# Kernel optimization log

Measured on AMD Instinct MI355X. Metric: run time of the kernel, lower is better.

The kernel has to match this reference:

```python
import jax, jax.numpy as jnp
import numpy as np

N = 100000          # total nodes
E = 3200000         # total edges (avg degree 32)
B = 100             # num graphs
NPG = N // B        # nodes per graph (uniform -> to_dense_batch is a reshape)
D_IN, D_H, D_E, N_CLS = 128, 64, 32, 10


def setup_inputs() -> dict:
    key = jax.random.key(0)
    ks = jax.random.split(key, 12)
    x = jax.random.normal(ks[0], (N, D_IN), jnp.float32)
    # edges strictly within each graph: offset by graph block
    epg = E // B
    offs = (jnp.arange(E, dtype=jnp.int32) // epg) * NPG
    src = jax.random.randint(ks[1], (E,), 0, NPG, jnp.int32) + offs
    dst = jax.random.randint(ks[2], (E,), 0, NPG, jnp.int32) + offs
    edge_index = jnp.stack([src, dst])
    batch = jnp.repeat(jnp.arange(B, dtype=jnp.int32), NPG)

    def glorot(k, fi, fo):
        return jax.random.normal(k, (fi, fo), jnp.float32) * (1.0 / np.sqrt(fi))

    return {
        "x": x, "edge_index": edge_index, "batch": batch,
        "W_a1": glorot(ks[3], D_IN, D_H), "b_a1": jnp.zeros((D_H,), jnp.float32),
        "W_a2": glorot(ks[4], D_H, D_E),  "b_a2": jnp.zeros((D_E,), jnp.float32),
        "W_x1": glorot(ks[5], D_IN, D_H), "b_x1": jnp.zeros((D_H,), jnp.float32),
        "W_x2": glorot(ks[6], D_H, D_E),  "b_x2": jnp.zeros((D_E,), jnp.float32),
        "W_lin": glorot(ks[7], D_E * D_E, N_CLS),
        "b_lin": jnp.zeros((N_CLS,), jnp.float32),
    }


def _gcn(x, W, b, src, dst, n):
    """PyG GCNConv(improved=True): sym-norm with self-loop weight 2."""
    h = x @ W                                                   # [n, out]
    deg = jax.ops.segment_sum(jnp.ones_like(dst, h.dtype), dst, n) + 2.0
    dinv = jax.lax.rsqrt(deg)                                   # [n]
    coef = dinv[src] * dinv[dst]                                # [E]
    agg = jax.ops.segment_sum(h[src] * coef[:, None], dst, n)   # gather-scatter
    agg = agg + (2.0 * dinv * dinv)[:, None] * h                # self-loop term
    return agg + b


def _segment_softmax(v, seg, nseg):
    m = jax.ops.segment_max(v, seg, nseg)
    e = jnp.exp(v - m[seg])
    s = jax.ops.segment_sum(e, seg, nseg)
    return e / s[seg]


def reference(x, edge_index, batch, W_a1, b_a1, W_a2, b_a2,
              W_x1, b_x1, W_x2, b_x2, W_lin, b_lin):
    src, dst = edge_index[0], edge_index[1]
    n = x.shape[0]
    a1 = jax.nn.relu(_gcn(x, W_a1, b_a1, src, dst, n))
    a2 = _segment_softmax(_gcn(a1, W_a2, b_a2, src, dst, n), batch, B)
    x1 = jax.nn.relu(_gcn(x, W_x1, b_x1, src, dst, n))
    x2 = jax.nn.relu(_gcn(x1, W_x2, b_x2, src, dst, n))
    # uniform graph sizes -> to_dense_batch is a reshape (no padding needed)
    a_b = a2.reshape(B, NPG, D_E)
    x_b = x2.reshape(B, NPG, D_E)
    prods = jnp.einsum('bne,bnf->bef', a_b, x_b)   # bmm(a^T, x): [B, D_E, D_E]
    flat = prods.reshape(B, D_E * D_E)
    return jax.nn.softmax(flat @ W_lin + b_lin, axis=-1)
```

## Files before the change

kernel.cpp:

```cpp
#include <hip/hip_runtime.h>
#include <hip/hip_bf16.h>
#include <hip/hip_fp16.h>

#define N_NODES 100000
#define N_EDGES 3200000
#define NB      100
#define NPG     1000
#define EPG     32000
#define DIN     128
#define DH      64
#define DE      32
#define NCLS    10
#define SORT_BLOCKS 104


typedef _Float16 h2_t __attribute__((ext_vector_type(2)));

__device__ __forceinline__ float dot2f(unsigned a, unsigned b, float c) {
#if __has_builtin(__builtin_amdgcn_fdot2)
    return __builtin_amdgcn_fdot2(__builtin_bit_cast(h2_t, a),
                                  __builtin_bit_cast(h2_t, b), c, false);
#else
    float d;
    asm("v_dot2_f32_f16 %0, %1, %2, %3" : "=v"(d) : "v"(a), "v"(b), "v"(c));
    return d;
#endif
}

#define DOT8(rA, rB, dv)                                                        \
    acc[0] = dot2f(__builtin_amdgcn_perm(rB.x, rA.x, 0x05040100u), dv, acc[0]); \
    acc[1] = dot2f(__builtin_amdgcn_perm(rB.x, rA.x, 0x07060302u), dv, acc[1]); \
    acc[2] = dot2f(__builtin_amdgcn_perm(rB.y, rA.y, 0x05040100u), dv, acc[2]); \
    acc[3] = dot2f(__builtin_amdgcn_perm(rB.y, rA.y, 0x07060302u), dv, acc[3]); \
    acc[4] = dot2f(__builtin_amdgcn_perm(rB.z, rA.z, 0x05040100u), dv, acc[4]); \
    acc[5] = dot2f(__builtin_amdgcn_perm(rB.z, rA.z, 0x07060302u), dv, acc[5]); \
    acc[6] = dot2f(__builtin_amdgcn_perm(rB.w, rA.w, 0x05040100u), dv, acc[6]); \
    acc[7] = dot2f(__builtin_amdgcn_perm(rB.w, rA.w, 0x07060302u), dv, acc[7]);


union SharedU {
    struct {
        __align__(16) unsigned short buf[EPG];
        int cnt[NPG];
        int pre[NPG];
        int sm[1024];
        unsigned short dh[NPG];
    } so;
    struct {
        float xs[4][32][128];
        float ws[32][128];
    } ge;
};

__global__ __launch_bounds__(1024) void k_sg(const int* __restrict__ src,
                                             const int* __restrict__ dst,
                                             const float* __restrict__ x,
                                             const float* __restrict__ Wa,
                                             const float* __restrict__ Wx,
                                             int* __restrict__ rowptr,
                                             float* __restrict__ dinv,
                                             unsigned int* __restrict__ esrc,
                                             unsigned short* __restrict__ h16) {
    __shared__ SharedU S;
    int t = threadIdx.x;
    if (blockIdx.x < SORT_BLOCKS) {
        int g = (blockIdx.x & 7) + 8 * (blockIdx.x >> 3);
        if (g >= NB) return;
        int ebase = g * EPG, nbase = g * NPG;
        if (t < NPG) S.so.cnt[t] = 0;
        __syncthreads();
        for (int i = t; i < EPG; i += 1024)
            atomicAdd(&S.so.cnt[dst[ebase + i] - nbase], 1);
        __syncthreads();
        int v = (t < NPG) ? S.so.cnt[t] : 0;
        if (t < NPG) {
            float dv = rsqrtf((float)v + 2.0f);
            dinv[nbase + t] = dv;
            S.so.dh[t] = __half_as_ushort(__float2half_rn(dv));
        }
        S.so.sm[t] = v;
        __syncthreads();
        for (int off = 1; off < 1024; off <<= 1) {
            int xx = (t >= off) ? S.so.sm[t - off] : 0;
            __syncthreads();
            S.so.sm[t] += xx;
            __syncthreads();
        }
        if (t < NPG) {
            int ex = S.so.sm[t] - v;
            S.so.pre[t] = ex;
            rowptr[nbase + t] = ebase + ex;
        }
        if (g == NB - 1 && t == 0) rowptr[N_NODES] = N_EDGES;
        __syncthreads();
        for (int i = t; i < EPG; i += 1024) {
            int e = ebase + i;
            int d = dst[e] - nbase;
            int s = src[e] - nbase;
            int pos = atomicAdd(&S.so.pre[d], 1);
            S.so.buf[pos] = (unsigned short)s;
        }
        __syncthreads();
        uint4* gout = (uint4*)(esrc + ebase);
        const ushort4* lbuf = (const ushort4*)S.so.buf;
        for (int i = t; i < EPG / 4; i += 1024) {
            ushort4 s4 = lbuf[i];
            uint4 o;
            o.x = ((unsigned)s4.x * 16) | ((unsigned)S.so.dh[s4.x] << 16);
            o.y = ((unsigned)s4.y * 16) | ((unsigned)S.so.dh[s4.y] << 16);
            o.z = ((unsigned)s4.z * 16) | ((unsigned)S.so.dh[s4.z] << 16);
            o.w = ((unsigned)s4.w * 16) | ((unsigned)S.so.dh[s4.w] << 16);
            gout[i] = o;
        }
    } else {
        int b = blockIdx.x - SORT_BLOCKS;
        int xcd = b & 7, slot = b >> 3;
        int g = xcd + 8 * (slot >> 3);
        int chunk = slot & 7;
        if (g >= NB) return;
        int q  = t >> 8;
        int tq = t & 255;
        int row0 = g * NPG + chunk * 128 + q * 32;
        for (int i = 0; i < 4; i++) {
            int idx = tq + 256 * i;
            int r = idx >> 5, k4 = idx & 31;
            int rr = row0 + r; if (rr >= N_NODES) rr = N_NODES - 1;
            *(float4*)&S.ge.xs[q][r][k4 * 4] = *(const float4*)&x[(size_t)rr * 128 + k4 * 4];
        }
        float acc[4][4] = {};
        int rg = tq >> 5, cg = tq & 31;
        for (int kt = 0; kt < 4; kt++) {
            __syncthreads();
            {
                int kk = t >> 5, c4 = t & 31;
                int k = kt * 32 + kk, c = c4 * 4;
                float4 v;
                if (c < 64) v = *(const float4*)&Wa[k * 64 + c];
                else        v = *(const float4*)&Wx[k * 64 + (c - 64)];
                *(float4*)&S.ge.ws[kk][c] = v;
            }
            __syncthreads();
            for (int kk = 0; kk < 32; kk++) {
                float4 w = *(float4*)&S.ge.ws[kk][cg * 4];
                float xv[4];
                for (int i = 0; i < 4; i++) xv[i] = S.ge.xs[q][rg * 4 + i][kt * 32 + kk];
                for (int i = 0; i < 4; i++) {
                    acc[i][0] += xv[i] * w.x; acc[i][1] += xv[i] * w.y;
                    acc[i][2] += xv[i] * w.z; acc[i][3] += xv[i] * w.w;
                }
            }
        }
        for (int i = 0; i < 4; i++) {
            int r = row0 + rg * 4 + i;
            if (r < N_NODES) {
                union { ushort4 u; __half2 h[2]; } pk;
                pk.h[0] = __floats2half2_rn(acc[i][0], acc[i][1]);
                pk.h[1] = __floats2half2_rn(acc[i][2], acc[i][3]);
                *(ushort4*)&h16[r * 128 + cg * 4] = pk.u;
            }
        }
    }
}


__global__ __launch_bounds__(256) void k_agg128(const unsigned short* __restrict__ h16,
                                                const int* __restrict__ rowptr,
                                                const unsigned int* __restrict__ esrc,
                                                const float* __restrict__ dinv,
                                                const float* __restrict__ ba,
                                                const float* __restrict__ bx,
                                                unsigned short* __restrict__ outB16) {
    int xcd = blockIdx.x & 7, slot = blockIdx.x >> 3;
    int gi = slot / 250, chunk = slot - gi * 250;
    int g = xcd + 8 * gi;
    if (g >= NB) return;
    int nl   = chunk * 4 + (threadIdx.x >> 6);
    int wid  = g * NPG + nl;
    int lane = threadIdx.x & 63;
    int sub = lane >> 4;
    int cl  = lane & 15;
    const uint4* hg4 = (const uint4*)(h16 + g * NPG * 128);
    float acc[8] = {};
    union U8 { uint4 u; __half h[8]; };
    int e0 = rowptr[wid], e1 = rowptr[wid + 1];
    int e = e0;
    for (; e + 16 <= e1; e += 16) {
        unsigned pv0 = esrc[e + sub];
        unsigned pv1 = esrc[e + 4 + sub];
        unsigned pv2 = esrc[e + 8 + sub];
        unsigned pv3 = esrc[e + 12 + sub];
        uint4 r0 = hg4[(pv0 & 0xffffu) + cl];
        uint4 r1 = hg4[(pv1 & 0xffffu) + cl];
        uint4 r2 = hg4[(pv2 & 0xffffu) + cl];
        uint4 r3 = hg4[(pv3 & 0xffffu) + cl];
        unsigned dA = __builtin_amdgcn_perm(pv1, pv0, 0x07060302u);
        unsigned dB = __builtin_amdgcn_perm(pv3, pv2, 0x07060302u);
        DOT8(r0, r1, dA);
        DOT8(r2, r3, dB);
    }
    for (; e + 8 <= e1; e += 8) {
        unsigned pv0 = esrc[e + sub];
        unsigned pv1 = esrc[e + 4 + sub];
        uint4 r0 = hg4[(pv0 & 0xffffu) + cl];
        uint4 r1 = hg4[(pv1 & 0xffffu) + cl];
        unsigned dA = __builtin_amdgcn_perm(pv1, pv0, 0x07060302u);
        DOT8(r0, r1, dA);
    }
    for (; e < e1; e += 4) {
        int ee = e + sub;
        unsigned pv; float scale;
        if (ee < e1) { pv = esrc[ee]; scale = 1.0f; }
        else         { pv = esrc[e];  scale = 0.0f; }
        U8 r; r.u = hg4[(pv & 0xffffu) + cl];
        float dv = scale * __half2float(__ushort_as_half((unsigned short)(pv >> 16)));
        #pragma unroll
        for (int k = 0; k < 8; k++)
            acc[k] += dv * __half2float(r.h[k]);
    }
    #pragma unroll
    for (int k = 0; k < 8; k++) {
        acc[k] += __shfl_xor(acc[k], 16);
        acc[k] += __shfl_xor(acc[k], 32);
    }
    if (sub == 0) {
        float di = dinv[wid];
        float sw = 2.0f * di * di;
        U8 hv; hv.u = hg4[nl * 16 + cl];
        int cl8 = cl * 8;
        const float* bb = (cl8 < 64) ? &ba[cl8] : &bx[cl8 - 64];
        union { __half2 h[4]; uint4 q; } pk;
        #pragma unroll
        for (int k = 0; k < 4; k++) {
            float ox = fmaxf(di * acc[2 * k]     + sw * __half2float(hv.h[2 * k])     + bb[2 * k],     0.0f);
            float oy = fmaxf(di * acc[2 * k + 1] + sw * __half2float(hv.h[2 * k + 1]) + bb[2 * k + 1], 0.0f);
            pk.h[k] = __floats2half2_rn(ox, oy);
        }
        *(uint4*)&outB16[wid * 128 + cl8] = pk.q;
    }
}


__global__ __launch_bounds__(256) void k_agg64(const unsigned short* __restrict__ g16,
                                               const int* __restrict__ rowptr,
                                               const unsigned int* __restrict__ esrc,
                                               const float* __restrict__ dinv,
                                               const float* __restrict__ ba2,
                                               const float* __restrict__ bx2,
                                               float* __restrict__ s2) {
    int xcd = blockIdx.x & 7, slot = blockIdx.x >> 3;
    int gi = slot / 250, chunk = slot - gi * 250;
    int g = xcd + 8 * gi;
    if (g >= NB) return;
    int nl   = chunk * 4 + (threadIdx.x >> 6);
    int wid  = g * NPG + nl;
    int lane = threadIdx.x & 63;
    int sub = lane >> 3;
    int cl  = lane & 7;
    const uint4* gg4 = (const uint4*)(g16 + g * NPG * 64);
    float acc[8] = {};
    union U8 { uint4 u; __half h[8]; };
    int e0 = rowptr[wid], e1 = rowptr[wid + 1];
    int e = e0;
    for (; e + 16 <= e1; e += 16) {
        unsigned pv0 = esrc[e + sub];
        unsigned pv1 = esrc[e + 8 + sub];
        uint4 r0 = gg4[((pv0 & 0xffffu) >> 1) + cl];
        uint4 r1 = gg4[((pv1 & 0xffffu) >> 1) + cl];
        unsigned dA = __builtin_amdgcn_perm(pv1, pv0, 0x07060302u);
        DOT8(r0, r1, dA);
    }
    for (; e < e1; e += 8) {
        int ee = e + sub;
        unsigned pv; float scale;
        if (ee < e1) { pv = esrc[ee]; scale = 1.0f; }
        else         { pv = esrc[e];  scale = 0.0f; }
        U8 r; r.u = gg4[((pv & 0xffffu) >> 1) + cl];
        float dv = scale * __half2float(__ushort_as_half((unsigned short)(pv >> 16)));
        #pragma unroll
        for (int k = 0; k < 8; k++)
            acc[k] += dv * __half2float(r.h[k]);
    }
    #pragma unroll
    for (int k = 0; k < 8; k++) {
        acc[k] += __shfl_xor(acc[k], 8);
        acc[k] += __shfl_xor(acc[k], 16);
        acc[k] += __shfl_xor(acc[k], 32);
    }
    if (sub == 0) {
        float di = dinv[wid];
        float sw = 2.0f * di * di;
        U8 hv; hv.u = gg4[nl * 8 + cl];
        int cl8 = cl * 8;
        float o[8];
        #pragma unroll
        for (int k = 0; k < 8; k++)
            o[k] = di * acc[k] + sw * __half2float(hv.h[k]);
        if (cl8 < 32) {
            #pragma unroll
            for (int k = 0; k < 8; k++) o[k] += ba2[cl8 + k];
        } else {
            #pragma unroll
            for (int k = 0; k < 8; k++) o[k] = fmaxf(o[k] + bx2[cl8 - 32 + k], 0.0f);
        }
        *(float4*)&s2[wid * 64 + cl8]     = make_float4(o[0], o[1], o[2], o[3]);
        *(float4*)&s2[wid * 64 + cl8 + 4] = make_float4(o[4], o[5], o[6], o[7]);
    }
}


__global__ __launch_bounds__(256) void k_gemm2(const unsigned short* __restrict__ Bm16,
                                               const float* __restrict__ Wa2,
                                               const float* __restrict__ Wx2,
                                               unsigned short* __restrict__ g16) {
    __shared__ float xs[64][132];
    __shared__ float ws[64][68];
    int xcd = blockIdx.x & 7, slot = blockIdx.x >> 3;
    int g = xcd + 8 * (slot >> 4);
    int chunk = slot & 15;
    if (g >= NB) return;
    int row0 = g * NPG + chunk * 64;
    int t = threadIdx.x;
    for (int i = 0; i < 4; i++) {
        int idx = t + 256 * i;
        int k = idx >> 4, c4 = idx & 15, c = c4 * 4;
        float4 v;
        if (c < 32) v = *(const float4*)&Wa2[k * 32 + c];
        else        v = *(const float4*)&Wx2[k * 32 + (c - 32)];
        *(float4*)&ws[k][c] = v;
    }
    for (int i = 0; i < 4; i++) {
        int idx = t + 256 * i;
        int r = idx >> 4, c8 = idx & 15;
        int rr = row0 + r; if (rr >= N_NODES) rr = N_NODES - 1;
        union { uint4 u; __half2 h[4]; } pk;
        pk.u = *(const uint4*)&Bm16[rr * 128 + c8 * 8];
        float2 f0 = __half22float2(pk.h[0]);
        float2 f1 = __half22float2(pk.h[1]);
        float2 f2 = __half22float2(pk.h[2]);
        float2 f3 = __half22float2(pk.h[3]);
        int cb = c8 * 8;
        *(float4*)&xs[r][cb]     = make_float4(f0.x, f0.y, f1.x, f1.y);
        *(float4*)&xs[r][cb + 4] = make_float4(f2.x, f2.y, f3.x, f3.y);
    }
    __syncthreads();
    int cg = t & 15, rg = t >> 4;
    int koff = (cg < 8) ? 0 : 64;
    float acc[4][4] = {};
    for (int k = 0; k < 64; k++) {
        float4 w = *(float4*)&ws[k][cg * 4];
        float xv[4];
        for (int i = 0; i < 4; i++) xv[i] = xs[rg * 4 + i][koff + k];
        for (int i = 0; i < 4; i++) {
            acc[i][0] += xv[i] * w.x; acc[i][1] += xv[i] * w.y;
            acc[i][2] += xv[i] * w.z; acc[i][3] += xv[i] * w.w;
        }
    }
    for (int i = 0; i < 4; i++) {
        int r = row0 + rg * 4 + i;
        if (r < N_NODES) {
            union { ushort4 u; __half2 h[2]; } pk;
            pk.h[0] = __floats2half2_rn(acc[i][0], acc[i][1]);
            pk.h[1] = __floats2half2_rn(acc[i][2], acc[i][3]);
            *(ushort4*)&g16[r * 64 + cg * 4] = pk.u;
        }
    }
}


__global__ __launch_bounds__(512) void k_smax(const float* __restrict__ s2,
                                              float* __restrict__ gmax,
                                              float* __restrict__ sinv) {
    __shared__ float red[16][32];
    int g = (blockIdx.x & 7) + 8 * (blockIdx.x >> 3);
    if (g >= NB) return;
    int t = threadIdx.x;
    int c = t & 31, sub = t >> 5;
    size_t base = (size_t)g * NPG;
    float m = -1e30f;
    for (int n = sub; n < NPG; n += 16)
        m = fmaxf(m, s2[(base + n) * 64 + c]);
    red[sub][c] = m; __syncthreads();
    if (sub == 0) {
        for (int j = 1; j < 16; j++) m = fmaxf(m, red[j][c]);
        red[0][c] = m;
        gmax[g * 32 + c] = m;
    }
    __syncthreads();
    m = red[0][c];
    __syncthreads();
    float sum = 0.0f;
    for (int n = sub; n < NPG; n += 16)
        sum += __expf(s2[(base + n) * 64 + c] - m);
    red[sub][c] = sum; __syncthreads();
    if (sub == 0) {
        for (int j = 1; j < 16; j++) sum += red[j][c];
        sinv[g * 32 + c] = 1.0f / sum;
    }
}


__global__ __launch_bounds__(256) void k_pool(const float* __restrict__ s2,
                                              const float* __restrict__ gmax,
                                              float* __restrict__ prods) {
    __shared__ float ta[25][32];
    __shared__ float tx[25][32];
    __shared__ float gm[32];
    int xcd = blockIdx.x & 7, slot = blockIdx.x >> 3;
    int g = xcd + 8 * (slot >> 3);
    int ch = slot & 7;
    if (g >= NB) return;
    int t = threadIdx.x;
    if (t < 32) gm[t] = gmax[g * 32 + t];
    int e  = t >> 3;
    int f4 = t & 7;
    float a0 = 0.f, a1 = 0.f, a2 = 0.f, a3 = 0.f;
    int base = g * NPG + ch * 125;
    for (int n0 = 0; n0 < 125; n0 += 25) {
        __syncthreads();
        for (int i = t; i < 25 * 16; i += 256) {
            int r = i >> 4, c4 = i & 15;
            float4 v = *(const float4*)&s2[(size_t)(base + n0 + r) * 64 + c4 * 4];
            if (c4 < 8) {
                int cb = c4 * 4;
                v.x = __expf(v.x - gm[cb + 0]);
                v.y = __expf(v.y - gm[cb + 1]);
                v.z = __expf(v.z - gm[cb + 2]);
                v.w = __expf(v.w - gm[cb + 3]);
                *(float4*)&ta[r][cb] = v;
            } else {
                *(float4*)&tx[r][(c4 - 8) * 4] = v;
            }
        }
        __syncthreads();
        #pragma unroll 5
        for (int n = 0; n < 25; n++) {
            float a   = ta[n][e];
            float4 xv = *(float4*)&tx[n][f4 * 4];
            a0 += a * xv.x; a1 += a * xv.y; a2 += a * xv.z; a3 += a * xv.w;
        }
    }
    *(float4*)&prods[((size_t)(g * 8 + ch)) * 1024 + e * 32 + f4 * 4] =
        make_float4(a0, a1, a2, a3);
}


__global__ __launch_bounds__(256) void k_head(const float* __restrict__ prods,
                                              const float* __restrict__ sinv,
                                              const float* __restrict__ Wlin,
                                              const float* __restrict__ blin,
                                              float* __restrict__ out) {
    __shared__ float red[4][NCLS];
    int g = (blockIdx.x & 7) + 8 * (blockIdx.x >> 3);
    if (g >= NB) return;
    int t = threadIdx.x;
    float p[NCLS];
    for (int c = 0; c < NCLS; c++) p[c] = 0.0f;
    const float* pg = &prods[(size_t)g * 8 * 1024];
    for (int j = 0; j < 4; j++) {
        int k = t * 4 + j;
        int e = k >> 5;
        float v = 0.0f;
        #pragma unroll
        for (int q = 0; q < 8; q++) v += pg[q * 1024 + k];
        v *= sinv[g * 32 + e];
        const float* wrow = &Wlin[k * NCLS];
        for (int c = 0; c < NCLS; c++) p[c] += v * wrow[c];
    }
    for (int off = 32; off > 0; off >>= 1)
        for (int c = 0; c < NCLS; c++) p[c] += __shfl_down(p[c], off, 64);
    int wave = t >> 6, lane = t & 63;
    if (lane == 0)
        for (int c = 0; c < NCLS; c++) red[wave][c] = p[c];
    __syncthreads();
    if (t == 0) {
        float logits[NCLS]; float mx = -1e30f;
        for (int c = 0; c < NCLS; c++) {
            logits[c] = red[0][c] + red[1][c] + red[2][c] + red[3][c] + blin[c];
            mx = fmaxf(mx, logits[c]);
        }
        float s = 0.0f;
        for (int c = 0; c < NCLS; c++) { logits[c] = expf(logits[c] - mx); s += logits[c]; }
        float inv = 1.0f / s;
        for (int c = 0; c < NCLS; c++) out[g * NCLS + c] = logits[c] * inv;
    }
}


extern "C" void kernel_launch(void* const* d_in, const int* in_sizes, int n_in,
                              void* d_out, int out_size, void* d_ws, size_t ws_size,
                              hipStream_t stream) {
    const float* x    = (const float*)d_in[0];
    const int*   ei   = (const int*)d_in[1];
    const float* Wa1  = (const float*)d_in[3];
    const float* ba1  = (const float*)d_in[4];
    const float* Wa2  = (const float*)d_in[5];
    const float* ba2  = (const float*)d_in[6];
    const float* Wx1  = (const float*)d_in[7];
    const float* bx1  = (const float*)d_in[8];
    const float* Wx2  = (const float*)d_in[9];
    const float* bx2  = (const float*)d_in[10];
    const float* Wlin = (const float*)d_in[11];
    const float* blin = (const float*)d_in[12];
    float* out = (float*)d_out;

    char* w = (char*)d_ws;
    auto alloc = [&](size_t bytes) -> void* {
        void* p = (void*)w;
        w += (bytes + 255) & ~(size_t)255;
        return p;
    };
    int*            rowptr = (int*)alloc((N_NODES + 1) * sizeof(int));
    float*          dinv   = (float*)alloc(N_NODES * sizeof(float));
    unsigned int*   esrc   = (unsigned int*)alloc((size_t)N_EDGES * sizeof(unsigned int));
    float*          gmax   = (float*)alloc(NB * DE * sizeof(float));
    float*          sinv   = (float*)alloc(NB * DE * sizeof(float));
    float*          prods  = (float*)alloc((size_t)NB * 8 * 1024 * sizeof(float));
    unsigned short* h16    = (unsigned short*)alloc((size_t)N_NODES * 128 * sizeof(unsigned short));
    unsigned short* b16    = (unsigned short*)alloc((size_t)N_NODES * 128 * sizeof(unsigned short));
    unsigned short* g16    = (unsigned short*)alloc((size_t)N_NODES * 64 * sizeof(unsigned short));
    float*          s2     = (float*)alloc((size_t)N_NODES * 64 * sizeof(float));

    const int* srcp = ei;
    const int* dstp = ei + N_EDGES;

    k_sg<<<SORT_BLOCKS + 8 * 13 * 8, 1024, 0, stream>>>(srcp, dstp, x, Wa1, Wx1,
                                                        rowptr, dinv, esrc, h16);
    k_agg128<<<8 * 13 * 250, 256, 0, stream>>>(h16, rowptr, esrc, dinv, ba1, bx1, b16);
    k_gemm2<<<8 * 13 * 16, 256, 0, stream>>>(b16, Wa2, Wx2, g16);
    k_agg64<<<8 * 13 * 250, 256, 0, stream>>>(g16, rowptr, esrc, dinv, ba2, bx2, s2);
    k_smax<<<8 * 13, 512, 0, stream>>>(s2, gmax, sinv);
    k_pool<<<8 * 13 * 8, 256, 0, stream>>>(s2, gmax, prods);
    k_head<<<8 * 13, 256, 0, stream>>>(prods, sinv, Wlin, blin, out);
}
```

Measured before the change: 328.5 us.

## Use f16 MFMA for first-layer node feature GEMM in k_sg

Result: faster. 311.2 us (-5.3%).

```diff
diff --git a/kernel.cpp b/kernel.cpp
--- a/kernel.cpp
+++ b/kernel.cpp
@@ -15,6 +15,8 @@
 
 
 typedef _Float16 h2_t __attribute__((ext_vector_type(2)));
+typedef _Float16 h8_t __attribute__((ext_vector_type(8)));
+typedef float    f4_t __attribute__((ext_vector_type(4)));
 
 __device__ __forceinline__ float dot2f(unsigned a, unsigned b, float c) {
 #if __has_builtin(__builtin_amdgcn_fdot2)
@@ -47,9 +49,8 @@
         unsigned short dh[NPG];
     } so;
     struct {
-        float xs[4][32][128];
-        float ws[32][128];
-    } ge;
+        __align__(16) unsigned short wt[128 * 128];
+    } w1;
 };
 
 __global__ __launch_bounds__(1024) void k_sg(const int* __restrict__ src,
@@ -115,48 +116,62 @@
     } else {
         int b = blockIdx.x - SORT_BLOCKS;
         int xcd = b & 7, slot = b >> 3;
-        int g = xcd + 8 * (slot >> 3);
-        int chunk = slot & 7;
+        int g = xcd + 8 * (slot >> 2);
+        int chunk = slot & 3;
         if (g >= NB) return;
-        int q  = t >> 8;
-        int tq = t & 255;
-        int row0 = g * NPG + chunk * 128 + q * 32;
-        for (int i = 0; i < 4; i++) {
-            int idx = tq + 256 * i;
-            int r = idx >> 5, k4 = idx & 31;
-            int rr = row0 + r; if (rr >= N_NODES) rr = N_NODES - 1;
-            *(float4*)&S.ge.xs[q][r][k4 * 4] = *(const float4*)&x[(size_t)rr * 128 + k4 * 4];
-        }
-        float acc[4][4] = {};
-        int rg = tq >> 5, cg = tq & 31;
-        for (int kt = 0; kt < 4; kt++) {
-            __syncthreads();
-            {
-                int kk = t >> 5, c4 = t & 31;
-                int k = kt * 32 + kk, c = c4 * 4;
-                float4 v;
-                if (c < 64) v = *(const float4*)&Wa[k * 64 + c];
-                else        v = *(const float4*)&Wx[k * 64 + (c - 64)];
-                *(float4*)&S.ge.ws[kk][c] = v;
+        int row0 = g * NPG + chunk * 250;
+        for (int j = 0; j < 4; j++) {
+            int idx = t + 1024 * j;
+            int k = idx >> 5, c = (idx & 31) * 4;
+            float4 v;
+            if (c < 64) v = *(const float4*)&Wa[k * 64 + c];
+            else        v = *(const float4*)&Wx[k * 64 + (c - 64)];
+            float vv[4] = {v.x, v.y, v.z, v.w};
+            #pragma unroll
+            for (int m = 0; m < 4; m++) {
+                int cc = c + m;
+                int byte = cc * 256 + ((k * 2) ^ ((cc & 7) << 4));
+                *(__half*)((char*)S.w1.wt + byte) = __float2half_rn(vv[m]);
             }
-            __syncthreads();
-            for (int kk = 0; kk < 32; kk++) {
-                float4 w = *(float4*)&S.ge.ws[kk][cg * 4];
-                float xv[4];
-                for (int i = 0; i < 4; i++) xv[i] = S.ge.xs[q][rg * 4 + i][kt * 32 + kk];
-                for (int i = 0; i < 4; i++) {
-                    acc[i][0] += xv[i] * w.x; acc[i][1] += xv[i] * w.y;
-                    acc[i][2] += xv[i] * w.z; acc[i][3] += xv[i] * w.w;
-                }
+        }
+        __syncthreads();
+        int w = t >> 6, l = t & 63;
+        int lr = l & 15, kq = l >> 4;
+        int rowA = row0 + w * 16 + lr;
+        int rA = rowA < N_NODES ? rowA : N_NODES - 1;
+        const float* xr = &x[(size_t)rA * 128];
+        h8_t a[4];
+        #pragma unroll
+        for (int kc = 0; kc < 4; kc++) {
+            float4 lo = *(const float4*)&xr[kc * 32 + kq * 8];
+            float4 hi = *(const float4*)&xr[kc * 32 + kq * 8 + 4];
+            h8_t av;
+            av[0] = (_Float16)lo.x; av[1] = (_Float16)lo.y;
+            av[2] = (_Float16)lo.z; av[3] = (_Float16)lo.w;
+            av[4] = (_Float16)hi.x; av[5] = (_Float16)hi.y;
+            av[6] = (_Float16)hi.z; av[7] = (_Float16)hi.w;
+            a[kc] = av;
+        }
+        f4_t acc[8] = {};
+        #pragma unroll
+        for (int kc = 0; kc < 4; kc++) {
+            #pragma unroll
+            for (int n = 0; n < 8; n++) {
+                int cc = n * 16 + lr;
+                int byte = cc * 256 + (((kc * 32 + kq * 8) * 2) ^ ((cc & 7) << 4));
+                h8_t bf = *(h8_t*)((char*)S.w1.wt + byte);
+                acc[n] = __builtin_amdgcn_mfma_f32_16x16x32_f16(a[kc], bf, acc[n], 0, 0, 0);
             }
         }
-        for (int i = 0; i < 4; i++) {
-            int r = row0 + rg * 4 + i;
-            if (r < N_NODES) {
-                union { ushort4 u; __half2 h[2]; } pk;
-                pk.h[0] = __floats2half2_rn(acc[i][0], acc[i][1]);
-                pk.h[1] = __floats2half2_rn(acc[i][2], acc[i][3]);
-                *(ushort4*)&h16[r * 128 + cg * 4] = pk.u;
+        int rowD = row0 + w * 16 + kq * 4;
+        #pragma unroll
+        for (int n = 0; n < 8; n++) {
+            #pragma unroll
+            for (int j = 0; j < 4; j++) {
+                int r = rowD + j;
+                if (r < N_NODES)
+                    h16[(size_t)r * 128 + n * 16 + lr] =
+                        __half_as_ushort(__float2half_rn(acc[n][j]));
             }
         }
     }
@@ -523,7 +538,7 @@
     const int* srcp = ei;
     const int* dstp = ei + N_EDGES;
 
-    k_sg<<<SORT_BLOCKS + 8 * 13 * 8, 1024, 0, stream>>>(srcp, dstp, x, Wa1, Wx1,
+    k_sg<<<SORT_BLOCKS + 8 * 13 * 4, 1024, 0, stream>>>(srcp, dstp, x, Wa1, Wx1,
                                                         rowptr, dinv, esrc, h16);
     k_agg128<<<8 * 13 * 250, 256, 0, stream>>>(h16, rowptr, esrc, dinv, ba1, bx1, b16);
     k_gemm2<<<8 * 13 * 16, 256, 0, stream>>>(b16, Wa2, Wx2, g16);
```
